# Optimization experiments

Hardware: AMD Instinct MI355X
Metric: run time of the kernel (lower is better)

## Reference

```python
import jax, jax.numpy as jnp
import numpy as np

EPSILON = 1e-06


def setup_inputs() -> dict:
    key = jax.random.key(0)
    k1, k2 = jax.random.split(key)
    logits = jax.random.normal(k1, (16, 2, 1024, 1024), dtype=jnp.float32)
    labels = jax.random.randint(k2, (16, 1, 1024, 1024), 0, 2, dtype=jnp.int32)
    return {"logits": logits, "labels": labels}


def reference(logits, labels):
    # Build one-hot targets: channel 0 = background (label==0), channel 1 = foreground.
    t = labels.astype(bool)                      # [B,1,H,W]
    targets = jnp.concatenate([jnp.logical_not(t), t], axis=1).astype(jnp.float32)  # [B,2,H,W]
    probs = jax.nn.softmax(logits, axis=1)       # softmax over class channel
    axes = tuple(range(2, logits.ndim))          # spatial axes (2,3)
    numerator = 2.0 * jnp.sum(targets * probs, axis=axes)               # [B,2]
    denominator = jnp.sum(probs * probs + targets * targets, axis=axes)  # [B,2]
    return 1.0 - jnp.mean(numerator / (denominator + EPSILON))
```

## Files before the change

kernel.cpp:

```cpp
#include <hip/hip_runtime.h>

constexpr int HW = 1024 * 1024;
constexpr int NB = 16;
constexpr float EPS = 1e-6f;
constexpr int BLOCKS_PER_BATCH = 128;
constexpr int THREADS = 256;
constexpr int NVEC    = HW / 4;
constexpr int TPB     = BLOCKS_PER_BATCH * THREADS;
constexpr int U       = NVEC / TPB;

__global__ __launch_bounds__(THREADS, 4) void dice_partial(
        const float* __restrict__ logits,
        const int*   __restrict__ labels,
        float*       __restrict__ ws) {
    const int b   = blockIdx.x >> 7;
    const int blk = blockIdx.x & 127;

    const float4* __restrict__ L0 = reinterpret_cast<const float4*>(logits + (size_t)b * 2 * HW);
    const float4* __restrict__ L1 = reinterpret_cast<const float4*>(logits + (size_t)b * 2 * HW + HW);
    const int4*   __restrict__ LB = reinterpret_cast<const int4*>(labels + (size_t)b * HW);

    const int base = blk * THREADS + threadIdx.x;

    float4 a[U], c[U];
    int4   t[U];
    #pragma unroll
    for (int u = 0; u < U; ++u) {
        const int i = base + u * TPB;
        a[u] = L0[i];
        c[u] = L1[i];
        t[u] = LB[i];
    }

    float sp = 0.f, spp = 0.f, st = 0.f, stp = 0.f;
    #pragma unroll
    for (int u = 0; u < U; ++u) {
        float p, tf;
        p = 1.f / (1.f + __expf(a[u].x - c[u].x)); tf = (float)t[u].x;
        sp += p; spp = fmaf(p, p, spp); st += tf; stp = fmaf(tf, p, stp);
        p = 1.f / (1.f + __expf(a[u].y - c[u].y)); tf = (float)t[u].y;
        sp += p; spp = fmaf(p, p, spp); st += tf; stp = fmaf(tf, p, stp);
        p = 1.f / (1.f + __expf(a[u].z - c[u].z)); tf = (float)t[u].z;
        sp += p; spp = fmaf(p, p, spp); st += tf; stp = fmaf(tf, p, stp);
        p = 1.f / (1.f + __expf(a[u].w - c[u].w)); tf = (float)t[u].w;
        sp += p; spp = fmaf(p, p, spp); st += tf; stp = fmaf(tf, p, stp);
    }

    #pragma unroll
    for (int off = 32; off > 0; off >>= 1) {
        sp  += __shfl_down(sp,  off);
        spp += __shfl_down(spp, off);
        st  += __shfl_down(st,  off);
        stp += __shfl_down(stp, off);
    }

    __shared__ float red[4][4];
    const int wave = threadIdx.x >> 6;
    const int lane = threadIdx.x & 63;
    if (lane == 0) {
        red[wave][0] = sp; red[wave][1] = spp; red[wave][2] = st; red[wave][3] = stp;
    }
    __syncthreads();
    if (threadIdx.x == 0) {
        float a0 = 0.f, a1 = 0.f, a2 = 0.f, a3 = 0.f;
        #pragma unroll
        for (int w = 0; w < 4; ++w) {
            a0 += red[w][0]; a1 += red[w][1]; a2 += red[w][2]; a3 += red[w][3];
        }
        atomicAdd(&ws[b * 4 + 0], a0);
        atomicAdd(&ws[b * 4 + 1], a1);
        atomicAdd(&ws[b * 4 + 2], a2);
        atomicAdd(&ws[b * 4 + 3], a3);
    }
}

__global__ void dice_final(const float* __restrict__ ws, float* __restrict__ out) {
    float local = 0.f;
    const int b = threadIdx.x;
    if (b < NB) {
        const float Sp  = ws[b * 4 + 0];
        const float Spp = ws[b * 4 + 1];
        const float St  = ws[b * 4 + 2];
        const float Stp = ws[b * 4 + 3];
        const float N = (float)HW;

        const float num1 = 2.f * Stp;
        const float den1 = Spp + St;
        const float num0 = 2.f * (N - St - Sp + Stp);
        const float den0 = (N - 2.f * Sp + Spp) + (N - St);

        local = num0 / (den0 + EPS) + num1 / (den1 + EPS);
    }
    #pragma unroll
    for (int off = 32; off > 0; off >>= 1) local += __shfl_down(local, off);
    if (threadIdx.x == 0) out[0] = 1.f - local / 32.f;
}

extern "C" void kernel_launch(void* const* d_in, const int* in_sizes, int n_in,
                              void* d_out, int out_size, void* d_ws, size_t ws_size,
                              hipStream_t stream) {
    const float* logits = (const float*)d_in[0];
    const int*   labels = (const int*)d_in[1];
    float* out = (float*)d_out;
    float* ws  = (float*)d_ws;

    hipMemsetAsync(ws, 0, NB * 4 * sizeof(float), stream);
    dice_partial<<<NB * BLOCKS_PER_BATCH, THREADS, 0, stream>>>(logits, labels, ws);
    dice_final<<<1, 64, 0, stream>>>(ws, out);
}
```

Baseline: 257.3 us.

## Use nontemporal loads, drop atomics and memset via per-block partials plus tree reduce

The streaming loads of logits and labels become nontemporal vector loads interleaved with compute, instead of buffering all U iterations in registers first. This lowers register pressure, and launch bounds rise to 8 waves per SIMD for more occupancy. The global atomics and the hipMemsetAsync are replaced by per-block partial writes, an extra per-batch reduction kernel, and a final kernel. This removes atomic contention and the memset launch but adds one more kernel launch.

```diff
diff --git a/kernel.cpp b/kernel.cpp
--- a/kernel.cpp
+++ b/kernel.cpp
@@ -8,42 +8,39 @@
 constexpr int NVEC    = HW / 4;
 constexpr int TPB     = BLOCKS_PER_BATCH * THREADS;
 constexpr int U       = NVEC / TPB;
+constexpr int NBLK    = NB * BLOCKS_PER_BATCH;
 
-__global__ __launch_bounds__(THREADS, 4) void dice_partial(
+typedef float f32x4 __attribute__((ext_vector_type(4)));
+typedef int   i32x4 __attribute__((ext_vector_type(4)));
+
+__global__ __launch_bounds__(THREADS, 8) void dice_partial(
         const float* __restrict__ logits,
         const int*   __restrict__ labels,
-        float*       __restrict__ ws) {
+        f32x4*       __restrict__ ws4) {
     const int b   = blockIdx.x >> 7;
     const int blk = blockIdx.x & 127;
 
-    const float4* __restrict__ L0 = reinterpret_cast<const float4*>(logits + (size_t)b * 2 * HW);
-    const float4* __restrict__ L1 = reinterpret_cast<const float4*>(logits + (size_t)b * 2 * HW + HW);
-    const int4*   __restrict__ LB = reinterpret_cast<const int4*>(labels + (size_t)b * HW);
+    const f32x4* __restrict__ L0 = reinterpret_cast<const f32x4*>(logits + (size_t)b * 2 * HW);
+    const f32x4* __restrict__ L1 = reinterpret_cast<const f32x4*>(logits + (size_t)b * 2 * HW + HW);
+    const i32x4* __restrict__ LB = reinterpret_cast<const i32x4*>(labels + (size_t)b * HW);
 
     const int base = blk * THREADS + threadIdx.x;
 
-    float4 a[U], c[U];
-    int4   t[U];
+    float sp = 0.f, spp = 0.f, st = 0.f, stp = 0.f;
+
     #pragma unroll
     for (int u = 0; u < U; ++u) {
         const int i = base + u * TPB;
-        a[u] = L0[i];
-        c[u] = L1[i];
-        t[u] = LB[i];
-    }
+        f32x4 a = __builtin_nontemporal_load(&L0[i]);
+        f32x4 c = __builtin_nontemporal_load(&L1[i]);
+        i32x4 t = __builtin_nontemporal_load(&LB[i]);
 
-    float sp = 0.f, spp = 0.f, st = 0.f, stp = 0.f;
-    #pragma unroll
-    for (int u = 0; u < U; ++u) {
-        float p, tf;
-        p = 1.f / (1.f + __expf(a[u].x - c[u].x)); tf = (float)t[u].x;
-        sp += p; spp = fmaf(p, p, spp); st += tf; stp = fmaf(tf, p, stp);
-        p = 1.f / (1.f + __expf(a[u].y - c[u].y)); tf = (float)t[u].y;
-        sp += p; spp = fmaf(p, p, spp); st += tf; stp = fmaf(tf, p, stp);
-        p = 1.f / (1.f + __expf(a[u].z - c[u].z)); tf = (float)t[u].z;
-        sp += p; spp = fmaf(p, p, spp); st += tf; stp = fmaf(tf, p, stp);
-        p = 1.f / (1.f + __expf(a[u].w - c[u].w)); tf = (float)t[u].w;
-        sp += p; spp = fmaf(p, p, spp); st += tf; stp = fmaf(tf, p, stp);
+        #pragma unroll
+        for (int k = 0; k < 4; ++k) {
+            const float p  = 1.f / (1.f + __expf(a[k] - c[k]));
+            const float tf = (float)t[k];
+            sp += p; spp = fmaf(p, p, spp); st += tf; stp = fmaf(tf, p, stp);
+        }
     }
 
     #pragma unroll
@@ -62,26 +59,39 @@
     }
     __syncthreads();
     if (threadIdx.x == 0) {
-        float a0 = 0.f, a1 = 0.f, a2 = 0.f, a3 = 0.f;
-        #pragma unroll
-        for (int w = 0; w < 4; ++w) {
-            a0 += red[w][0]; a1 += red[w][1]; a2 += red[w][2]; a3 += red[w][3];
-        }
-        atomicAdd(&ws[b * 4 + 0], a0);
-        atomicAdd(&ws[b * 4 + 1], a1);
-        atomicAdd(&ws[b * 4 + 2], a2);
-        atomicAdd(&ws[b * 4 + 3], a3);
+        f32x4 r;
+        r.x = red[0][0] + red[1][0] + red[2][0] + red[3][0];
+        r.y = red[0][1] + red[1][1] + red[2][1] + red[3][1];
+        r.z = red[0][2] + red[1][2] + red[2][2] + red[3][2];
+        r.w = red[0][3] + red[1][3] + red[2][3] + red[3][3];
+        ws4[blockIdx.x] = r;
     }
 }
 
-__global__ void dice_final(const float* __restrict__ ws, float* __restrict__ out) {
-    float local = 0.f;
-    const int b = threadIdx.x;
-    if (b < NB) {
-        const float Sp  = ws[b * 4 + 0];
-        const float Spp = ws[b * 4 + 1];
-        const float St  = ws[b * 4 + 2];
-        const float Stp = ws[b * 4 + 3];
+__global__ __launch_bounds__(128) void dice_batch(
+        const f32x4* __restrict__ ws4,
+        float*       __restrict__ terms) {
+    const int b = blockIdx.x;
+    f32x4 v = ws4[b * BLOCKS_PER_BATCH + threadIdx.x];
+
+    #pragma unroll
+    for (int off = 32; off > 0; off >>= 1) {
+        v.x += __shfl_down(v.x, off);
+        v.y += __shfl_down(v.y, off);
+        v.z += __shfl_down(v.z, off);
+        v.w += __shfl_down(v.w, off);
+    }
+
+    __shared__ f32x4 red[2];
+    const int wave = threadIdx.x >> 6;
+    const int lane = threadIdx.x & 63;
+    if (lane == 0) red[wave] = v;
+    __syncthreads();
+    if (threadIdx.x == 0) {
+        const float Sp  = red[0].x + red[1].x;
+        const float Spp = red[0].y + red[1].y;
+        const float St  = red[0].z + red[1].z;
+        const float Stp = red[0].w + red[1].w;
         const float N = (float)HW;
 
         const float num1 = 2.f * Stp;
@@ -89,8 +99,12 @@
         const float num0 = 2.f * (N - St - Sp + Stp);
         const float den0 = (N - 2.f * Sp + Spp) + (N - St);
 
-        local = num0 / (den0 + EPS) + num1 / (den1 + EPS);
+        terms[b] = num0 / (den0 + EPS) + num1 / (den1 + EPS);
     }
+}
+
+__global__ void dice_final(const float* __restrict__ terms, float* __restrict__ out) {
+    float local = (threadIdx.x < NB) ? terms[threadIdx.x] : 0.f;
     #pragma unroll
     for (int off = 32; off > 0; off >>= 1) local += __shfl_down(local, off);
     if (threadIdx.x == 0) out[0] = 1.f - local / 32.f;
@@ -101,10 +115,11 @@
                               hipStream_t stream) {
     const float* logits = (const float*)d_in[0];
     const int*   labels = (const int*)d_in[1];
-    float* out = (float*)d_out;
-    float* ws  = (float*)d_ws;
+    float* out   = (float*)d_out;
+    f32x4* ws4   = (f32x4*)d_ws;
+    float* terms = (float*)d_ws + NBLK * 4;
 
-    hipMemsetAsync(ws, 0, NB * 4 * sizeof(float), stream);
-    dice_partial<<<NB * BLOCKS_PER_BATCH, THREADS, 0, stream>>>(logits, labels, ws);
-    dice_final<<<1, 64, 0, stream>>>(ws, out);
+    dice_partial<<<NBLK, THREADS, 0, stream>>>(logits, labels, ws4);
+    dice_batch<<<NB, 128, 0, stream>>>(ws4, terms);
+    dice_final<<<1, 64, 0, stream>>>(terms, out);
 }
```

After: 221.1 us. 14.1% less time.
